# Performance work log

Hardware: AMD Instinct MI355X
Metric: run time of the kernel (lower is better)

Reference implementation:

```python
import jax, jax.numpy as jnp
import numpy as np
import itertools

N_ELEC = 128
BOX_L = 10.0
DIM = 3
BATCH = 4096


def gen_kpoints(N, L, dim):
    # Faithful numpy port of genKpoints (FermiNet make_kpoints variant).
    rec = 2.0 * np.pi / L
    dk = 1.0 + 1e-05
    max_k = int((N * dk) ** (1.0 / dim) + 0.5)
    ordinals = sorted(range(-max_k, max_k + 1), key=abs)
    ords = np.array(list(itertools.product(ordinals, repeat=dim)), dtype=np.float64)
    kpoints = ords * rec
    order = np.argsort(np.linalg.norm(kpoints, axis=1), kind='stable')
    kpoints = kpoints[order]
    return kpoints[:N].astype(np.float32)


def make_switches(kpoints, dim):
    # Select cos for k-points on the 'positive' side, sin(-k.r) for the rest.
    weights = 10.0 ** np.arange(1, dim + 1)
    weighted_sums = np.sign(kpoints).dot(weights)
    k_signs = np.sign(weighted_sums + 1.0)
    cos_switch = ((k_signs + 1.0) / 2.0).astype(np.float32)
    sin_switch = ((1.0 - k_signs) / 2.0).astype(np.float32)
    return cos_switch, sin_switch


def setup_inputs() -> dict:
    key = jax.random.key(0)
    rs = jax.random.uniform(key, (BATCH, N_ELEC, DIM), dtype=jnp.float32) * BOX_L
    kpoints = gen_kpoints(N_ELEC, BOX_L, DIM)
    cos_switch, sin_switch = make_switches(kpoints, DIM)
    return {
        'rs': rs,
        'kpoints': jnp.asarray(kpoints),
        'cos_switch': jnp.asarray(cos_switch),
        'sin_switch': jnp.asarray(sin_switch),
    }


def reference(rs, kpoints, cos_switch, sin_switch):
    # dots[b, i, m] = k_m . r_{b,i}   -> [B, N, N]
    dots = jnp.einsum('bnd,md->bnm', rs, kpoints)
    # Slater matrix: rows = particles, cols = plane-wave orbitals.
    slater = cos_switch * jnp.cos(dots) + sin_switch * jnp.sin(-dots)
    # log |det| per walker (batched LU) -> [B]
    return jnp.linalg.slogdet(slater)[1]
```

## Files before the change

### kernel.cpp

```cpp
#include <hip/hip_runtime.h>
#include <stdint.h>

#define NM 128
#define NT 1024

typedef float v2f __attribute__((ext_vector_type(2)));

__device__ __forceinline__ float readlane_f(float v, int lane) {
    return __int_as_float(__builtin_amdgcn_readlane(__float_as_int(v), lane));
}

__device__ __forceinline__ unsigned wave_max_dpp(unsigned x) {
    int v = (int)x;
#define DPP_STEP(ctrl) \
    { int o = __builtin_amdgcn_update_dpp(0, v, ctrl, 0xf, 0xf, true); \
      v = ((unsigned)o > (unsigned)v) ? o : v; }
    DPP_STEP(0x111)
    DPP_STEP(0x112)
    DPP_STEP(0x114)
    DPP_STEP(0x118)
    DPP_STEP(0x142)
    DPP_STEP(0x143)
#undef DPP_STEP
    return (unsigned)v;
}

__device__ __forceinline__ unsigned pack_key(float v, int r) {
    return (((__float_as_uint(v) & 0x7fffffffu) >> 6) << 7) | (unsigned)r;
}

__device__ __forceinline__ unsigned argmax_bcast(unsigned ka, unsigned kb) {
    const unsigned m = wave_max_dpp(ka > kb ? ka : kb);
    return (unsigned)__builtin_amdgcn_readlane((int)m, 63);
}

__device__ __forceinline__ float sel_readlane(v2f c, int p) {
    return (p < 64) ? readlane_f(c.x, p) : readlane_f(c.y, p - 64);
}

__device__ __forceinline__ void factor8(v2f (&sv)[8], bool& elim0, bool& elim1,
                                        int r0, int r1, int l, int g,
                                        float2 (*colvg)[64],
                                        unsigned* keysF, float* pivsF,
                                        ulonglong2* masks) {
    const bool e0in = elim0, e1in = elim1;
    __builtin_amdgcn_s_setprio(1);
#pragma unroll
    for (int i = 0; i < 8; ++i) {
        const v2f c = sv[i];
        const unsigned key = argmax_bcast(elim0 ? 0u : pack_key(c.x, r0),
                                          elim1 ? 0u : pack_key(c.y, r1));
        const int pu = __builtin_amdgcn_readfirstlane((int)(key & 127u));
        const float piv = sel_readlane(c, pu);
        const float rcp = __builtin_amdgcn_rcpf(piv);
        elim0 = elim0 || (r0 == pu);
        elim1 = elim1 || (r1 == pu);
        const v2f lm = { elim0 ? 0.0f : c.x * rcp,
                         elim1 ? 0.0f : c.y * rcp };
        colvg[i][l] = make_float2(lm.x, lm.y);
        float u[8];
        if (pu < 64) {
#pragma unroll
            for (int m = i + 1; m < 8; ++m) u[m] = readlane_f(sv[m].x, pu);
        } else {
#pragma unroll
            for (int m = i + 1; m < 8; ++m) u[m] = readlane_f(sv[m].y, pu - 64);
        }
#pragma unroll
        for (int m = i + 1; m < 8; ++m)
            sv[m] = __builtin_elementwise_fma((v2f){-u[m], -u[m]}, lm, sv[m]);
        if (l == 0) { keysF[8 * g + i] = key; pivsF[8 * g + i] = piv; }
    }
    __builtin_amdgcn_s_setprio(0);
    const unsigned long long b0 = __ballot(elim0 && !e0in);
    const unsigned long long b1 = __ballot(elim1 && !e1in);
    if (l == 0) masks[g] = make_ulonglong2(b0, b1);
}

__device__ __forceinline__ void decode_p(const unsigned* keysR, int (&p)[8]) {
    const uint4 ka = *(const uint4*)&keysR[0];
    const uint4 kb = *(const uint4*)&keysR[4];
    p[0] = __builtin_amdgcn_readfirstlane((int)(ka.x & 127u));
    p[1] = __builtin_amdgcn_readfirstlane((int)(ka.y & 127u));
    p[2] = __builtin_amdgcn_readfirstlane((int)(ka.z & 127u));
    p[3] = __builtin_amdgcn_readfirstlane((int)(ka.w & 127u));
    p[4] = __builtin_amdgcn_readfirstlane((int)(kb.x & 127u));
    p[5] = __builtin_amdgcn_readfirstlane((int)(kb.y & 127u));
    p[6] = __builtin_amdgcn_readfirstlane((int)(kb.z & 127u));
    p[7] = __builtin_amdgcn_readfirstlane((int)(kb.w & 127u));
}

__global__ __launch_bounds__(NT, 8)
void slater_logdet(const float* __restrict__ rs,
                   const float* __restrict__ kpts,
                   const float* __restrict__ csw,
                   const float* __restrict__ ssw,
                   float* __restrict__ out) {
    __shared__ float2 colv[2][8][64];
    __shared__ unsigned keysF[NM];
    __shared__ float    pivsF[NM];
    __shared__ ulonglong2 masks[NM / 8];
    __shared__ float    redf[2];

    const int t  = threadIdx.x;
    const int b  = blockIdx.x;
    const int w  = t >> 6;
    const int l  = t & 63;
    const int r0 = l, r1 = l + 64;

    v2f sv[8];
    {
        const float x0 = rs[(b * NM + r0) * 3 + 0];
        const float y0 = rs[(b * NM + r0) * 3 + 1];
        const float z0 = rs[(b * NM + r0) * 3 + 2];
        const float x1 = rs[(b * NM + r1) * 3 + 0];
        const float y1 = rs[(b * NM + r1) * 3 + 1];
        const float z1 = rs[(b * NM + r1) * 3 + 2];
#pragma unroll
        for (int j = 0; j < 8; ++j) {
            const int m = 8 * w + j;
            const float kx = kpts[m * 3 + 0], ky = kpts[m * 3 + 1], kz = kpts[m * 3 + 2];
            const float cw = csw[m], sw = ssw[m];
            float sn, cn;
            __sincosf(kx * x0 + ky * y0 + kz * z0, &sn, &cn);
            sv[j].x = cw * cn - sw * sn;
            __sincosf(kx * x1 + ky * y1 + kz * z1, &sn, &cn);
            sv[j].y = cw * cn - sw * sn;
        }
    }

    bool elim0 = false, elim1 = false;

    if (w == 0)
        factor8(sv, elim0, elim1, r0, r1, l, 0, colv[0], keysF, pivsF, masks);
    __syncthreads();

    for (int rd = 0; rd < 15; ++rd) {
        if (w > rd) {
            const ulonglong2 mk = masks[rd];
            elim0 = elim0 || (((mk.x >> l) & 1ull) != 0);
            elim1 = elim1 || (((mk.y >> l) & 1ull) != 0);

            int p[8];
            decode_p(&keysF[8 * rd], p);
            const float2 (*cp)[64] = colv[rd & 1];
#pragma unroll
            for (int i = 0; i < 8; ++i) {
                const float2 la = cp[i][l];
                const v2f lm = (v2f){la.x, la.y};
                float u[8];
                if (p[i] < 64) {
#pragma unroll
                    for (int j = 0; j < 8; ++j) u[j] = readlane_f(sv[j].x, p[i]);
                } else {
#pragma unroll
                    for (int j = 0; j < 8; ++j) u[j] = readlane_f(sv[j].y, p[i] - 64);
                }
#pragma unroll
                for (int j = 0; j < 8; ++j)
                    sv[j] = __builtin_elementwise_fma((v2f){-u[j], -u[j]}, lm, sv[j]);
            }

            if (w == rd + 1)
                factor8(sv, elim0, elim1, r0, r1, l, rd + 1,
                        colv[(rd + 1) & 1], keysF, pivsF, masks);
        }
        __syncthreads();
    }

    float lg = 0.0f;
    if (t < NM) {
        lg = __logf(fabsf(pivsF[t]));
#pragma unroll
        for (int off = 32; off > 0; off >>= 1)
            lg += __shfl_xor(lg, off, 64);
        if ((t & 63) == 0) redf[t >> 6] = lg;
    }
    __syncthreads();
    if (t == 0) out[b] = redf[0] + redf[1];
}

extern "C" void kernel_launch(void* const* d_in, const int* in_sizes, int n_in,
                              void* d_out, int out_size, void* d_ws, size_t ws_size,
                              hipStream_t stream) {
    const float* rs = (const float*)d_in[0];
    const float* kp = (const float*)d_in[1];
    const float* cs = (const float*)d_in[2];
    const float* ss = (const float*)d_in[3];
    float* out = (float*)d_out;
    const int batch = in_sizes[0] / (NM * 3);
    slater_logdet<<<dim3(batch), dim3(NT), 0, stream>>>(rs, kp, cs, ss, out);
}
```

Measured before the change: 414.0 us.

## Replace per-round block barriers with atomic-counter dataflow between waves

Drops the 15 block-wide __syncthreads rounds. Each wave now polls a shared LDS counter and applies each factored panel as soon as the owning wave publishes it, then factors its own panel and bumps the counter. Every panel's multipliers get their own LDS slot (15 instead of 2 double-buffered) so producers never wait for consumers. This removes barrier stalls and lets waves pipeline, at the cost of more LDS per block (about 60KB), which can lower occupancy, plus spin-wait overhead.

```diff
diff --git a/kernel.cpp b/kernel.cpp
--- a/kernel.cpp
+++ b/kernel.cpp
@@ -96,11 +96,12 @@
                    const float* __restrict__ csw,
                    const float* __restrict__ ssw,
                    float* __restrict__ out) {
-    __shared__ float2 colv[2][8][64];
+    __shared__ float2 colv[15][8][64];
     __shared__ unsigned keysF[NM];
     __shared__ float    pivsF[NM];
-    __shared__ ulonglong2 masks[NM / 8];
+    __shared__ ulonglong2 masks[16];
     __shared__ float    redf[2];
+    __shared__ int      gcount;
 
     const int t  = threadIdx.x;
     const int b  = blockIdx.x;
@@ -129,44 +130,55 @@
         }
     }
 
+    if (t == 0) gcount = 0;
+    __syncthreads();
+
     bool elim0 = false, elim1 = false;
 
-    if (w == 0)
-        factor8(sv, elim0, elim1, r0, r1, l, 0, colv[0], keysF, pivsF, masks);
+    int applied = 0;
+    while (applied < w) {
+        const int avail = __hip_atomic_load(&gcount, __ATOMIC_ACQUIRE,
+                                            __HIP_MEMORY_SCOPE_WORKGROUP);
+        const int lim = avail < w ? avail : w;
+        if (lim > applied) {
+            do {
+                const int g = applied;
+                const ulonglong2 mk = masks[g];
+                elim0 = elim0 || (((mk.x >> l) & 1ull) != 0);
+                elim1 = elim1 || (((mk.y >> l) & 1ull) != 0);
+                int p[8];
+                decode_p(&keysF[8 * g], p);
+                float2 la[8];
+#pragma unroll
+                for (int i = 0; i < 8; ++i) la[i] = colv[g][i][l];
+#pragma unroll
+                for (int i = 0; i < 8; ++i) {
+                    const v2f lm = (v2f){la[i].x, la[i].y};
+                    float u[8];
+                    if (p[i] < 64) {
+#pragma unroll
+                        for (int j = 0; j < 8; ++j) u[j] = readlane_f(sv[j].x, p[i]);
+                    } else {
+#pragma unroll
+                        for (int j = 0; j < 8; ++j) u[j] = readlane_f(sv[j].y, p[i] - 64);
+                    }
+#pragma unroll
+                    for (int j = 0; j < 8; ++j)
+                        sv[j] = __builtin_elementwise_fma((v2f){-u[j], -u[j]}, lm, sv[j]);
+                }
+                ++applied;
+            } while (applied < lim);
+        } else if (w - avail > 1) {
+            __builtin_amdgcn_s_sleep(1);
+        }
+    }
+
+    factor8(sv, elim0, elim1, r0, r1, l, w,
+            colv[w < 15 ? w : 0], keysF, pivsF, masks);
+    __hip_atomic_store(&gcount, w + 1, __ATOMIC_RELEASE,
+                       __HIP_MEMORY_SCOPE_WORKGROUP);
+
     __syncthreads();
-
-    for (int rd = 0; rd < 15; ++rd) {
-        if (w > rd) {
-            const ulonglong2 mk = masks[rd];
-            elim0 = elim0 || (((mk.x >> l) & 1ull) != 0);
-            elim1 = elim1 || (((mk.y >> l) & 1ull) != 0);
-
-            int p[8];
-            decode_p(&keysF[8 * rd], p);
-            const float2 (*cp)[64] = colv[rd & 1];
-#pragma unroll
-            for (int i = 0; i < 8; ++i) {
-                const float2 la = cp[i][l];
-                const v2f lm = (v2f){la.x, la.y};
-                float u[8];
-                if (p[i] < 64) {
-#pragma unroll
-                    for (int j = 0; j < 8; ++j) u[j] = readlane_f(sv[j].x, p[i]);
-                } else {
-#pragma unroll
-                    for (int j = 0; j < 8; ++j) u[j] = readlane_f(sv[j].y, p[i] - 64);
-                }
-#pragma unroll
-                for (int j = 0; j < 8; ++j)
-                    sv[j] = __builtin_elementwise_fma((v2f){-u[j], -u[j]}, lm, sv[j]);
-            }
-
-            if (w == rd + 1)
-                factor8(sv, elim0, elim1, r0, r1, l, rd + 1,
-                        colv[(rd + 1) & 1], keysF, pivsF, masks);
-        }
-        __syncthreads();
-    }
 
     float lg = 0.0f;
     if (t < NM) {
```

Result: no change. 414.0 us (-0.0%).

## Process two matrices per block with mirrored column-panel assignment to balance waves

Applied to the files above, without the earlier changes.

Each block now factors two walkers' Slater matrices. Matrix A's column panels go to waves in ascending order and matrix B's in descending order, so each wave does roughly the same total trailing-update work and the triangular idle time of the blocked right-looking LU is filled. The change doubles register state per thread (16 v2f columns), doubles the shared buffers and halves the grid size. It risks higher register pressure and lower occupancy, and relies on the batch size being even.

```diff
diff --git a/kernel.cpp b/kernel.cpp
--- a/kernel.cpp
+++ b/kernel.cpp
@@ -38,16 +38,17 @@
     return (p < 64) ? readlane_f(c.x, p) : readlane_f(c.y, p - 64);
 }
 
-__device__ __forceinline__ void factor8(v2f (&sv)[8], bool& elim0, bool& elim1,
+template<int B>
+__device__ __forceinline__ void factor8(v2f (&sv)[16], bool& elim0, bool& elim1,
                                         int r0, int r1, int l, int g,
                                         float2 (*colvg)[64],
-                                        unsigned* keysF, float* pivsF,
-                                        ulonglong2* masks) {
+                                        unsigned* keysM, float* pivsM,
+                                        ulonglong2* masksM) {
     const bool e0in = elim0, e1in = elim1;
     __builtin_amdgcn_s_setprio(1);
 #pragma unroll
     for (int i = 0; i < 8; ++i) {
-        const v2f c = sv[i];
+        const v2f c = sv[B + i];
         const unsigned key = argmax_bcast(elim0 ? 0u : pack_key(c.x, r0),
                                           elim1 ? 0u : pack_key(c.y, r1));
         const int pu = __builtin_amdgcn_readfirstlane((int)(key & 127u));
@@ -61,20 +62,20 @@
         float u[8];
         if (pu < 64) {
 #pragma unroll
-            for (int m = i + 1; m < 8; ++m) u[m] = readlane_f(sv[m].x, pu);
+            for (int m = i + 1; m < 8; ++m) u[m] = readlane_f(sv[B + m].x, pu);
         } else {
 #pragma unroll
-            for (int m = i + 1; m < 8; ++m) u[m] = readlane_f(sv[m].y, pu - 64);
+            for (int m = i + 1; m < 8; ++m) u[m] = readlane_f(sv[B + m].y, pu - 64);
         }
 #pragma unroll
         for (int m = i + 1; m < 8; ++m)
-            sv[m] = __builtin_elementwise_fma((v2f){-u[m], -u[m]}, lm, sv[m]);
-        if (l == 0) { keysF[8 * g + i] = key; pivsF[8 * g + i] = piv; }
+            sv[B + m] = __builtin_elementwise_fma((v2f){-u[m], -u[m]}, lm, sv[B + m]);
+        if (l == 0) { keysM[8 * g + i] = key; pivsM[8 * g + i] = piv; }
     }
     __builtin_amdgcn_s_setprio(0);
     const unsigned long long b0 = __ballot(elim0 && !e0in);
     const unsigned long long b1 = __ballot(elim1 && !e1in);
-    if (l == 0) masks[g] = make_ulonglong2(b0, b1);
+    if (l == 0) masksM[g] = make_ulonglong2(b0, b1);
 }
 
 __device__ __forceinline__ void decode_p(const unsigned* keysR, int (&p)[8]) {
@@ -90,94 +91,123 @@
     p[7] = __builtin_amdgcn_readfirstlane((int)(kb.w & 127u));
 }
 
+template<int B>
+__device__ __forceinline__ void apply8(v2f (&sv)[16], const int (&p)[8],
+                                       const float2 (*cp)[64], int l) {
+#pragma unroll
+    for (int i = 0; i < 8; ++i) {
+        const float2 la = cp[i][l];
+        const v2f lm = (v2f){la.x, la.y};
+        float u[8];
+        if (p[i] < 64) {
+#pragma unroll
+            for (int j = 0; j < 8; ++j) u[j] = readlane_f(sv[B + j].x, p[i]);
+        } else {
+#pragma unroll
+            for (int j = 0; j < 8; ++j) u[j] = readlane_f(sv[B + j].y, p[i] - 64);
+        }
+#pragma unroll
+        for (int j = 0; j < 8; ++j)
+            sv[B + j] = __builtin_elementwise_fma((v2f){-u[j], -u[j]}, lm, sv[B + j]);
+    }
+}
+
 __global__ __launch_bounds__(NT, 8)
 void slater_logdet(const float* __restrict__ rs,
                    const float* __restrict__ kpts,
                    const float* __restrict__ csw,
                    const float* __restrict__ ssw,
                    float* __restrict__ out) {
-    __shared__ float2 colv[2][8][64];
-    __shared__ unsigned keysF[NM];
-    __shared__ float    pivsF[NM];
-    __shared__ ulonglong2 masks[NM / 8];
-    __shared__ float    redf[2];
+    __shared__ float2 colv[2][2][8][64];
+    __shared__ unsigned keysF[2][NM];
+    __shared__ float    pivsF[2][NM];
+    __shared__ ulonglong2 masks[2][16];
+    __shared__ float    redf[4];
 
     const int t  = threadIdx.x;
-    const int b  = blockIdx.x;
+    const int bA = 2 * blockIdx.x;
+    const int bB = 2 * blockIdx.x + 1;
     const int w  = t >> 6;
     const int l  = t & 63;
     const int r0 = l, r1 = l + 64;
 
-    v2f sv[8];
+    v2f sv[16];
     {
-        const float x0 = rs[(b * NM + r0) * 3 + 0];
-        const float y0 = rs[(b * NM + r0) * 3 + 1];
-        const float z0 = rs[(b * NM + r0) * 3 + 2];
-        const float x1 = rs[(b * NM + r1) * 3 + 0];
-        const float y1 = rs[(b * NM + r1) * 3 + 1];
-        const float z1 = rs[(b * NM + r1) * 3 + 2];
-#pragma unroll
-        for (int j = 0; j < 8; ++j) {
-            const int m = 8 * w + j;
+        const float* rsA = rs + (size_t)bA * NM * 3;
+        const float* rsB = rs + (size_t)bB * NM * 3;
+        const float ax0 = rsA[r0 * 3 + 0], ay0 = rsA[r0 * 3 + 1], az0 = rsA[r0 * 3 + 2];
+        const float ax1 = rsA[r1 * 3 + 0], ay1 = rsA[r1 * 3 + 1], az1 = rsA[r1 * 3 + 2];
+        const float bx0 = rsB[r0 * 3 + 0], by0 = rsB[r0 * 3 + 1], bz0 = rsB[r0 * 3 + 2];
+        const float bx1 = rsB[r1 * 3 + 0], by1 = rsB[r1 * 3 + 1], bz1 = rsB[r1 * 3 + 2];
+#pragma unroll
+        for (int j = 0; j < 16; ++j) {
+            const int m = (j < 8) ? (8 * w + j) : (8 * (15 - w) + (j - 8));
             const float kx = kpts[m * 3 + 0], ky = kpts[m * 3 + 1], kz = kpts[m * 3 + 2];
             const float cw = csw[m], sw = ssw[m];
             float sn, cn;
-            __sincosf(kx * x0 + ky * y0 + kz * z0, &sn, &cn);
-            sv[j].x = cw * cn - sw * sn;
-            __sincosf(kx * x1 + ky * y1 + kz * z1, &sn, &cn);
-            sv[j].y = cw * cn - sw * sn;
-        }
-    }
-
-    bool elim0 = false, elim1 = false;
+            if (j < 8) {
+                __sincosf(kx * ax0 + ky * ay0 + kz * az0, &sn, &cn);
+                sv[j].x = cw * cn - sw * sn;
+                __sincosf(kx * ax1 + ky * ay1 + kz * az1, &sn, &cn);
+                sv[j].y = cw * cn - sw * sn;
+            } else {
+                __sincosf(kx * bx0 + ky * by0 + kz * bz0, &sn, &cn);
+                sv[j].x = cw * cn - sw * sn;
+                __sincosf(kx * bx1 + ky * by1 + kz * bz1, &sn, &cn);
+                sv[j].y = cw * cn - sw * sn;
+            }
+        }
+    }
+
+    bool eA0 = false, eA1 = false, eB0 = false, eB1 = false;
 
     if (w == 0)
-        factor8(sv, elim0, elim1, r0, r1, l, 0, colv[0], keysF, pivsF, masks);
+        factor8<0>(sv, eA0, eA1, r0, r1, l, 0, colv[0][0],
+                   keysF[0], pivsF[0], masks[0]);
+    if (w == 15)
+        factor8<8>(sv, eB0, eB1, r0, r1, l, 0, colv[1][0],
+                   keysF[1], pivsF[1], masks[1]);
     __syncthreads();
 
     for (int rd = 0; rd < 15; ++rd) {
-        if (w > rd) {
-            const ulonglong2 mk = masks[rd];
-            elim0 = elim0 || (((mk.x >> l) & 1ull) != 0);
-            elim1 = elim1 || (((mk.y >> l) & 1ull) != 0);
-
+        const int par = rd & 1;
+        if (rd < w) {
+            const ulonglong2 mk = masks[0][rd];
+            eA0 = eA0 || (((mk.x >> l) & 1ull) != 0);
+            eA1 = eA1 || (((mk.y >> l) & 1ull) != 0);
             int p[8];
-            decode_p(&keysF[8 * rd], p);
-            const float2 (*cp)[64] = colv[rd & 1];
-#pragma unroll
-            for (int i = 0; i < 8; ++i) {
-                const float2 la = cp[i][l];
-                const v2f lm = (v2f){la.x, la.y};
-                float u[8];
-                if (p[i] < 64) {
-#pragma unroll
-                    for (int j = 0; j < 8; ++j) u[j] = readlane_f(sv[j].x, p[i]);
-                } else {
-#pragma unroll
-                    for (int j = 0; j < 8; ++j) u[j] = readlane_f(sv[j].y, p[i] - 64);
-                }
-#pragma unroll
-                for (int j = 0; j < 8; ++j)
-                    sv[j] = __builtin_elementwise_fma((v2f){-u[j], -u[j]}, lm, sv[j]);
-            }
-
-            if (w == rd + 1)
-                factor8(sv, elim0, elim1, r0, r1, l, rd + 1,
-                        colv[(rd + 1) & 1], keysF, pivsF, masks);
+            decode_p(&keysF[0][8 * rd], p);
+            apply8<0>(sv, p, colv[0][par], l);
+            if (rd == w - 1)
+                factor8<0>(sv, eA0, eA1, r0, r1, l, rd + 1,
+                           colv[0][(rd + 1) & 1], keysF[0], pivsF[0], masks[0]);
+        }
+        if (rd < 15 - w) {
+            const ulonglong2 mk = masks[1][rd];
+            eB0 = eB0 || (((mk.x >> l) & 1ull) != 0);
+            eB1 = eB1 || (((mk.y >> l) & 1ull) != 0);
+            int p[8];
+            decode_p(&keysF[1][8 * rd], p);
+            apply8<8>(sv, p, colv[1][par], l);
+            if (rd == 14 - w)
+                factor8<8>(sv, eB0, eB1, r0, r1, l, rd + 1,
+                           colv[1][(rd + 1) & 1], keysF[1], pivsF[1], masks[1]);
         }
         __syncthreads();
     }
 
     float lg = 0.0f;
-    if (t < NM) {
-        lg = __logf(fabsf(pivsF[t]));
+    if (t < 256) {
+        const int mat = t >> 7;
+        lg = __logf(fabsf(pivsF[mat][t & 127]));
 #pragma unroll
         for (int off = 32; off > 0; off >>= 1)
             lg += __shfl_xor(lg, off, 64);
         if ((t & 63) == 0) redf[t >> 6] = lg;
     }
     __syncthreads();
-    if (t == 0) out[b] = redf[0] + redf[1];
+    if (t == 0) out[bA] = redf[0] + redf[1];
+    if (t == 1) out[bB] = redf[2] + redf[3];
 }
 
 extern "C" void kernel_launch(void* const* d_in, const int* in_sizes, int n_in,
@@ -189,5 +219,5 @@
     const float* ss = (const float*)d_in[3];
     float* out = (float*)d_out;
     const int batch = in_sizes[0] / (NM * 3);
-    slater_logdet<<<dim3(batch), dim3(NT), 0, stream>>>(rs, kp, cs, ss, out);
-}
+    slater_logdet<<<dim3(batch / 2), dim3(NT), 0, stream>>>(rs, kp, cs, ss, out);
+}
```

Measured after the change: 388.8 us. 1.06x faster.
